# Optimization experiments

Hardware: AMD Instinct MI355X
Metric: run time of the kernel (lower is better)

Reference implementation:

```python
import jax, jax.numpy as jnp
import numpy as np

NEG_SLOPE = 0.01  # nn.LeakyReLU default
NUM_GRAPHS = 64


def leaky_relu(x):
    return jnp.where(x >= 0, x, NEG_SLOPE * x)


def gcn_conv(x, edge_index, W, b):
    """PyG GCNConv: add self-loops, symmetric norm, aggregate, + bias."""
    n = x.shape[0]
    h = x @ W  # [N, F]
    loop = jnp.arange(n, dtype=edge_index.dtype)
    src = jnp.concatenate([edge_index[0], loop])
    dst = jnp.concatenate([edge_index[1], loop])
    deg = jax.ops.segment_sum(jnp.ones_like(dst, dtype=h.dtype), dst, num_segments=n)
    dinv = jnp.where(deg > 0, deg ** -0.5, 0.0)
    norm = dinv[src] * dinv[dst]  # [E+N]
    msg = h[src] * norm[:, None]  # [E+N, F] dominant intermediate
    out = jax.ops.segment_sum(msg, dst, num_segments=n)
    return out + b


def gep(x, batch, num_graphs):
    """global mean pool over batch segment ids."""
    s = jax.ops.segment_sum(x, batch, num_segments=num_graphs)
    cnt = jax.ops.segment_sum(jnp.ones(x.shape[0], dtype=x.dtype), batch, num_segments=num_graphs)
    return s / jnp.maximum(cnt, 1.0)[:, None]


def setup_inputs() -> dict:
    key = jax.random.key(0)
    ks = jax.random.split(key, 16)
    N, E, F, D, B = 10000, 80000, 1024, 128, NUM_GRAPHS
    sc = 1.0 / np.sqrt(F)
    inp = {
        "pro1_x": jax.random.normal(ks[0], (N, F), jnp.float32),
        "pro1_edge_index": jax.random.randint(ks[1], (2, E), 0, N, jnp.int64),
        "pro1_batch": jnp.sort(jax.random.randint(ks[2], (N,), 0, B, jnp.int64)),
        "pro2_x": jax.random.normal(ks[3], (N, F), jnp.float32),
        "pro2_edge_index": jax.random.randint(ks[4], (2, E), 0, N, jnp.int64),
        "pro2_batch": jnp.sort(jax.random.randint(ks[5], (N,), 0, B, jnp.int64)),
        "mas1_straight": 0, "mas1_flipped": 0, "mas2_straight": 0, "mas2_flipped": 0,
        "conv1_W": jax.random.normal(ks[6], (F, F), jnp.float32) * sc,
        "conv1_b": jnp.zeros((F,), jnp.float32),
        "fc1_W": jax.random.normal(ks[7], (F, D), jnp.float32) * sc,
        "fc1_b": jnp.zeros((D,), jnp.float32),
        "conv2_W": jax.random.normal(ks[8], (F, F), jnp.float32) * sc,
        "conv2_b": jnp.zeros((F,), jnp.float32),
        "fc2_W": jax.random.normal(ks[9], (F, D), jnp.float32) * sc,
        "fc2_b": jnp.zeros((D,), jnp.float32),
        "final_W": jax.random.normal(ks[10], (2 * D, 1), jnp.float32) * (1.0 / np.sqrt(2 * D)),
        "final_b": jnp.zeros((1,), jnp.float32),
    }
    return inp


def reference(pro1_x, pro1_edge_index, pro1_batch, pro2_x, pro2_edge_index, pro2_batch,
              mas1_straight, mas1_flipped, mas2_straight, mas2_flipped,
              conv1_W, conv1_b, fc1_W, fc1_b, conv2_W, conv2_b, fc2_W, fc2_b,
              final_W, final_b):
    # branch 1 (dropout = identity at inference)
    x = leaky_relu(gcn_conv(pro1_x, pro1_edge_index, conv1_W, conv1_b))
    x = gep(x, pro1_batch, NUM_GRAPHS)
    x = leaky_relu(x @ fc1_W + fc1_b)
    # branch 2
    xt = leaky_relu(gcn_conv(pro2_x, pro2_edge_index, conv2_W, conv2_b))
    xt = gep(xt, pro2_batch, NUM_GRAPHS)
    xt = leaky_relu(xt @ fc2_W + fc2_b)
    combined = jnp.concatenate([x, xt], axis=1)  # [B, 256]
    return combined @ final_W + final_b  # [B, 1]
```

## Files before the change

### kernel.cpp

```cpp
#include <hip/hip_runtime.h>
#include <cstdint>
#include <cstddef>

#define FDIM 1024
#define DDIM 128
#define NGRAPH 64
#define FCH 8
#define QN 4
#define FILLB 320

#define AS1 __attribute__((address_space(1)))
#define AS3 __attribute__((address_space(3)))

typedef float f32x4 __attribute__((ext_vector_type(4)));
typedef short s16x8 __attribute__((ext_vector_type(8)));
typedef unsigned short u16x8 __attribute__((ext_vector_type(8)));

__device__ __forceinline__ unsigned short f2bf(float f) {
  unsigned int x = __float_as_uint(f);
  unsigned int r = (x + 0x7fffu + ((x >> 16) & 1u)) >> 16;
  return (unsigned short)r;
}
__device__ __forceinline__ float bflo(unsigned int v) {
  return __uint_as_float(v << 16);
}
__device__ __forceinline__ float bfhi(unsigned int v) {
  return __uint_as_float(v & 0xffff0000u);
}

__device__ __forceinline__ int lower_bound(const int* a, int n, int v) {
  int lo = 0, hi = n;
  while (lo < hi) {
    int mid = (lo + hi) >> 1;
    if (a[mid] < v) lo = mid + 1; else hi = mid;
  }
  return lo;
}

__global__ __launch_bounds__(256) void k_prep_cast(const int* __restrict__ ei1,
                                                   const int* __restrict__ ei2,
                                                   int* deg1, int* deg2,
                                                   const float4* __restrict__ x1,
                                                   const float4* __restrict__ x2,
                                                   const float* __restrict__ W1,
                                                   const float* __restrict__ W2,
                                                   u16x8* xb1, u16x8* xb2,
                                                   unsigned short* Wt1, unsigned short* Wt2,
                                                   int E, int n8, int gE, int nxb) {
  __shared__ unsigned short tile[64][65];
  int br = blockIdx.y;
  int x = blockIdx.x, t = threadIdx.x;
  if (x < gE) {
    const int* ei = br ? ei2 : ei1;
    int* deg = br ? deg2 : deg1;
    int i = x * 256 + t;
    if (i < E) atomicAdd(&deg[ei[E + i]], 1);
  } else if (x < gE + nxb) {
    const float4* xx = br ? x2 : x1;
    u16x8* xb = br ? xb2 : xb1;
    int i = (x - gE) * 256 + t;
    if (i < n8) {
      float4 v0 = xx[2 * i];
      float4 v1 = xx[2 * i + 1];
      u16x8 o;
      o[0] = f2bf(v0.x); o[1] = f2bf(v0.y); o[2] = f2bf(v0.z); o[3] = f2bf(v0.w);
      o[4] = f2bf(v1.x); o[5] = f2bf(v1.y); o[6] = f2bf(v1.z); o[7] = f2bf(v1.w);
      xb[i] = o;
    }
  } else {
    const float* W = br ? W2 : W1;
    unsigned short* Wt = br ? Wt2 : Wt1;
    int tid16 = x - gE - nxb;
    int kb = tid16 >> 4, nb = tid16 & 15;
    int tn = t & 63, tg = t >> 6;
    #pragma unroll
    for (int r = 0; r < 16; ++r) {
      int kk = tg * 16 + r;
      tile[kk][tn] = f2bf(W[(size_t)(kb * 64 + kk) * FDIM + nb * 64 + tn]);
    }
    __syncthreads();
    #pragma unroll
    for (int r = 0; r < 16; ++r) {
      int nn = tg * 16 + r;
      Wt[(size_t)(nb * 64 + nn) * FDIM + kb * 64 + tn] = tile[tn][nn];
    }
  }
}

#define SCAN_T 1024
#define SCAN_PER 16
__global__ __launch_bounds__(SCAN_T) void k_scan(const int* __restrict__ deg1,
                                                 const int* __restrict__ deg2,
                                                 int* off1, int* off2,
                                                 int* cur1, int* cur2,
                                                 float* dinv1, float* dinv2,
                                                 const int* __restrict__ batch1,
                                                 const int* __restrict__ batch2,
                                                 int* cnt1, int* gstart1,
                                                 int* cnt2, int* gstart2, int n) {
  if (blockIdx.x == 2) {
    int t = threadIdx.x;
    if (t < 128) {
      const int* batch = (t < NGRAPH) ? batch1 : batch2;
      int* cnt = (t < NGRAPH) ? cnt1 : cnt2;
      int* gstart = (t < NGRAPH) ? gstart1 : gstart2;
      int g = t & (NGRAPH - 1);
      int lo = lower_bound(batch, n, g);
      int hi = lower_bound(batch, n, g + 1);
      gstart[g] = lo;
      cnt[g] = hi - lo;
    }
    return;
  }
  const int* deg = blockIdx.x ? deg2 : deg1;
  int* off = blockIdx.x ? off2 : off1;
  int* cur = blockIdx.x ? cur2 : cur1;
  float* dinv = blockIdx.x ? dinv2 : dinv1;
  __shared__ int sums[SCAN_T];
  int t = threadIdx.x;
  int base = t * SCAN_PER;
  int local[SCAN_PER];
  int s = 0;
  #pragma unroll
  for (int i = 0; i < SCAN_PER; ++i) {
    int idx = base + i;
    int d = (idx < n) ? (deg[idx] + 1) : 0;
    local[i] = s;
    s += d;
    if (idx < n) dinv[idx] = rsqrtf((float)d);
  }
  sums[t] = s;
  __syncthreads();
  for (int o = 1; o < SCAN_T; o <<= 1) {
    int v = (t >= o) ? sums[t - o] : 0;
    __syncthreads();
    sums[t] += v;
    __syncthreads();
  }
  int basesum = (t > 0) ? sums[t - 1] : 0;
  #pragma unroll
  for (int i = 0; i < SCAN_PER; ++i) {
    int idx = base + i;
    if (idx < n) { int o = basesum + local[i]; off[idx] = o; cur[idx] = o; }
  }
  if (t == SCAN_T - 1) off[n] = sums[SCAN_T - 1];
}

__global__ __launch_bounds__(256, 3) void k_fill_gemm(const int* __restrict__ ei1,
                                                      const int* __restrict__ ei2,
                                                      int* cur1, int* cur2,
                                                      const float* __restrict__ dinv1,
                                                      const float* __restrict__ dinv2,
                                                      int* adjsrc1, int* adjsrc2,
                                                      float* adjw1, float* adjw2,
                                                      const unsigned short* __restrict__ A1,
                                                      const unsigned short* __restrict__ A2,
                                                      const unsigned short* __restrict__ B1,
                                                      const unsigned short* __restrict__ B2,
                                                      unsigned short* __restrict__ C1,
                                                      unsigned short* __restrict__ C2,
                                                      int E, int N, int M) {
  __shared__ unsigned short sm[8192];
  int br = blockIdx.y;
  if (blockIdx.x < FILLB) {
    const int* ei = br ? ei2 : ei1;
    int* cur = br ? cur2 : cur1;
    const float* dinv = br ? dinv2 : dinv1;
    int* adjsrc = br ? adjsrc2 : adjsrc1;
    float* adjw = br ? adjw2 : adjw1;
    int i = blockIdx.x * 256 + threadIdx.x;
    if (i < E) {
      int s = ei[i];
      int d = ei[E + i];
      int p = atomicAdd(&cur[d], 1);
      adjsrc[p] = s;
      adjw[p] = dinv[s] * dinv[d];
    }
    if (i < N) {
      int p = atomicAdd(&cur[i], 1);
      adjsrc[p] = i;
      adjw[p] = dinv[i] * dinv[i];
    }
    return;
  }
  const unsigned short* A = br ? A2 : A1;
  const unsigned short* Bt = br ? B2 : B1;
  unsigned short* C = br ? C2 : C1;
  const int K = FDIM;
  int tid = threadIdx.x;
  int w = tid >> 6, lane = tid & 63;
  int wm = w >> 1, wn = w & 1;

  int bx = blockIdx.x - FILLB;
  int per_xcd = (gridDim.x - FILLB) >> 3;
  int l = (bx & 7) * per_xcd + (bx >> 3);
  int m0 = (l >> 3) * 128;
  int n0 = (l & 7) * 128;

  int sub = lane >> 2;
  int kq = lane & 3;

  f32x4 acc[4][4];
  #pragma unroll
  for (int i = 0; i < 4; ++i)
    #pragma unroll
    for (int j = 0; j < 4; ++j)
      acc[i][j] = (f32x4){0.f, 0.f, 0.f, 0.f};

  for (int k0 = 0; k0 < K; k0 += 32) {
    #pragma unroll
    for (int j = 0; j < 2; ++j) {
      int chunk = w * 2 + j;
      int ra = m0 + chunk * 16 + sub;
      if (ra > M - 1) ra = M - 1;
      const unsigned short* ga = A + (size_t)ra * K + k0 + kq * 8;
      __builtin_amdgcn_global_load_lds((const AS1 unsigned int*)ga,
                                       (AS3 unsigned int*)&sm[chunk * 512], 16, 0, 0);
      int rb = n0 + chunk * 16 + sub;
      const unsigned short* gb = Bt + (size_t)rb * K + k0 + kq * 8;
      __builtin_amdgcn_global_load_lds((const AS1 unsigned int*)gb,
                                       (AS3 unsigned int*)&sm[4096 + chunk * 512], 16, 0, 0);
    }
    __syncthreads();
    s16x8 af[4], bfr[4];
    #pragma unroll
    for (int i = 0; i < 4; ++i) {
      int rowa = wm * 64 + i * 16 + (lane & 15);
      af[i] = *(const s16x8*)&sm[rowa * 32 + (lane >> 4) * 8];
      int rowb = wn * 64 + i * 16 + (lane & 15);
      bfr[i] = *(const s16x8*)&sm[4096 + rowb * 32 + (lane >> 4) * 8];
    }
    #pragma unroll
    for (int i = 0; i < 4; ++i)
      #pragma unroll
      for (int j = 0; j < 4; ++j)
        acc[i][j] = __builtin_amdgcn_mfma_f32_16x16x32_bf16(af[i], bfr[j], acc[i][j], 0, 0, 0);
    __syncthreads();
  }

  #pragma unroll
  for (int i = 0; i < 4; ++i) {
    int row_base = m0 + wm * 64 + i * 16 + (lane >> 4) * 4;
    #pragma unroll
    for (int j = 0; j < 4; ++j) {
      int col = n0 + wn * 64 + j * 16 + (lane & 15);
      #pragma unroll
      for (int r = 0; r < 4; ++r) {
        int row = row_base + r;
        if (row < M) C[(size_t)row * FDIM + col] = f2bf(acc[i][j][r]);
      }
    }
  }
}

__global__ __launch_bounds__(256) void k_aggpool(const unsigned short* __restrict__ h1,
                                                 const unsigned short* __restrict__ h2,
                                                 const int* __restrict__ off1,
                                                 const int* __restrict__ off2,
                                                 const int* __restrict__ adjsrc1,
                                                 const int* __restrict__ adjsrc2,
                                                 const float* __restrict__ adjw1,
                                                 const float* __restrict__ adjw2,
                                                 const float* __restrict__ bias1,
                                                 const float* __restrict__ bias2,
                                                 const int* __restrict__ cnt1,
                                                 const int* __restrict__ cnt2,
                                                 const int* __restrict__ gstart1,
                                                 const int* __restrict__ gstart2,
                                                 float* pool4_1, float* pool4_2) {
  int br = blockIdx.y;
  const unsigned short* h = br ? h2 : h1;
  const int* off = br ? off2 : off1;
  const int* adjsrc = br ? adjsrc2 : adjsrc1;
  const float* adjw = br ? adjw2 : adjw1;
  const float* bias = br ? bias2 : bias1;
  const int* cnt = br ? cnt2 : cnt1;
  const int* gstart = br ? gstart2 : gstart1;
  float* pool4 = br ? pool4_2 : pool4_1;

  int x = blockIdx.x;
  int chunk = x & (FCH - 1);
  int r = x >> 3;
  int g = r & (NGRAPH - 1);
  int q = r >> 6;

  int t = threadIdx.x;
  int grp = t >> 6, lane = t & 63;

  int n = cnt[g];
  int start = gstart[g];
  int per = (n + QN - 1) / QN;
  int v0 = start + q * per;
  int v1 = min(start + n, v0 + per);

  int colbase = chunk * 128 + lane * 2;
  const unsigned short* hc = h + colbase;
  float2 b2 = *(const float2*)(bias + colbase);
  float s0 = 0.f, s1 = 0.f;

  for (int v = v0 + grp; v < v1; v += 4) {
    int pb = off[v], pe = off[v + 1];
    float a0 = 0.f, a1 = 0.f;
    for (int pbb = pb; pbb < pe; pbb += 64) {
      int m = min(64, pe - pbb);
      int lp = pbb + ((lane < m) ? lane : (m - 1));
      int vs = adjsrc[lp];
      float vw = adjw[lp];
      int j = 0;
      for (; j + 4 <= m; j += 4) {
        int i0 = __shfl(vs, j),     i1 = __shfl(vs, j + 1);
        int i2 = __shfl(vs, j + 2), i3 = __shfl(vs, j + 3);
        float w0 = __shfl(vw, j),     w1 = __shfl(vw, j + 1);
        float w2 = __shfl(vw, j + 2), w3 = __shfl(vw, j + 3);
        unsigned int h0 = *(const unsigned int*)(hc + ((size_t)i0 << 10));
        unsigned int hv1 = *(const unsigned int*)(hc + ((size_t)i1 << 10));
        unsigned int hv2 = *(const unsigned int*)(hc + ((size_t)i2 << 10));
        unsigned int hv3 = *(const unsigned int*)(hc + ((size_t)i3 << 10));
        a0 += w0 * bflo(h0);  a1 += w0 * bfhi(h0);
        a0 += w1 * bflo(hv1); a1 += w1 * bfhi(hv1);
        a0 += w2 * bflo(hv2); a1 += w2 * bfhi(hv2);
        a0 += w3 * bflo(hv3); a1 += w3 * bfhi(hv3);
      }
      for (; j < m; ++j) {
        int i0 = __shfl(vs, j);
        float w0 = __shfl(vw, j);
        unsigned int h0 = *(const unsigned int*)(hc + ((size_t)i0 << 10));
        a0 += w0 * bflo(h0);
        a1 += w0 * bfhi(h0);
      }
    }
    a0 += b2.x; a1 += b2.y;
    s0 += (a0 >= 0.f) ? a0 : 0.01f * a0;
    s1 += (a1 >= 0.f) ? a1 : 0.01f * a1;
  }

  __shared__ float sm[4][128];
  sm[grp][lane * 2] = s0;
  sm[grp][lane * 2 + 1] = s1;
  __syncthreads();
  if (t < 128) {
    float sum = sm[0][t] + sm[1][t] + sm[2][t] + sm[3][t];
    float ic = 1.0f / fmaxf((float)n, 1.0f);
    pool4[((size_t)(q * NGRAPH + g)) * FDIM + chunk * 128 + t] = sum * ic;
  }
}

__global__ __launch_bounds__(256) void k_fc_final(const float* __restrict__ pool4_1,
                                                  const float* __restrict__ pool4_2,
                                                  const float* __restrict__ W1,
                                                  const float* __restrict__ W2,
                                                  const float* __restrict__ b1,
                                                  const float* __restrict__ b2,
                                                  const float* __restrict__ fW,
                                                  const float* __restrict__ fb,
                                                  float* __restrict__ out) {
  int g = blockIdx.x;
  int t = threadIdx.x;
  int half = t >> 7;
  int j = t & 127;
  const float* pool4 = half ? pool4_2 : pool4_1;
  const float* W = half ? W2 : W1;
  const float* b = half ? b2 : b1;
  __shared__ float xs[2][FDIM];
  for (int k = j; k < FDIM; k += DDIM) {
    float v = 0.f;
    #pragma unroll
    for (int q = 0; q < QN; ++q)
      v += pool4[((size_t)(q * NGRAPH + g)) * FDIM + k];
    xs[half][k] = v;
  }
  __syncthreads();
  float acc = b[j];
  for (int k = 0; k < FDIM; ++k) acc += xs[half][k] * W[(size_t)k * DDIM + j];
  acc = (acc >= 0.f) ? acc : 0.01f * acc;
  float c = acc * fW[half * DDIM + j];
  #pragma unroll
  for (int o = 32; o > 0; o >>= 1) c += __shfl_down(c, o);
  __shared__ float ws[4];
  if ((t & 63) == 0) ws[t >> 6] = c;
  __syncthreads();
  if (t == 0) out[g] = ws[0] + ws[1] + ws[2] + ws[3] + fb[0];
}

extern "C" void kernel_launch(void* const* d_in, const int* in_sizes, int n_in,
                              void* d_out, int out_size, void* d_ws, size_t ws_size,
                              hipStream_t stream) {
  const float* x1 = (const float*)d_in[0];
  const int* ei1 = (const int*)d_in[1];
  const int* batch1 = (const int*)d_in[2];
  const float* x2 = (const float*)d_in[3];
  const int* ei2 = (const int*)d_in[4];
  const int* batch2 = (const int*)d_in[5];
  const float* conv1_W = (const float*)d_in[10];
  const float* conv1_b = (const float*)d_in[11];
  const float* fc1_W = (const float*)d_in[12];
  const float* fc1_b = (const float*)d_in[13];
  const float* conv2_W = (const float*)d_in[14];
  const float* conv2_b = (const float*)d_in[15];
  const float* fc2_W = (const float*)d_in[16];
  const float* fc2_b = (const float*)d_in[17];
  const float* final_W = (const float*)d_in[18];
  const float* final_b = (const float*)d_in[19];
  float* out = (float*)d_out;

  const int N = in_sizes[2];
  const int E = in_sizes[1] / 2;
  const int A = E + N;

  size_t off_b = 0;
  auto alloc = [&](size_t bytes) -> void* {
    void* p = (char*)d_ws + off_b;
    off_b += (bytes + 255) & ~(size_t)255;
    return p;
  };
  unsigned short* xbf1 = (unsigned short*)alloc((size_t)N * FDIM * 2);
  unsigned short* xbf2 = (unsigned short*)alloc((size_t)N * FDIM * 2);
  unsigned short* hbf1 = (unsigned short*)alloc((size_t)N * FDIM * 2);
  unsigned short* hbf2 = (unsigned short*)alloc((size_t)N * FDIM * 2);
  unsigned short* Wt1 = (unsigned short*)alloc((size_t)FDIM * FDIM * 2);
  unsigned short* Wt2 = (unsigned short*)alloc((size_t)FDIM * FDIM * 2);
  int* deg1 = (int*)alloc(N * 4);
  int* deg2 = (int*)alloc(N * 4);
  int* cnt1 = (int*)alloc(NGRAPH * 4);
  int* cnt2 = (int*)alloc(NGRAPH * 4);
  int* gstart1 = (int*)alloc(NGRAPH * 4);
  int* gstart2 = (int*)alloc(NGRAPH * 4);
  int* off1 = (int*)alloc((N + 1) * 4);
  int* off2 = (int*)alloc((N + 1) * 4);
  int* cur1 = (int*)alloc(N * 4);
  int* cur2 = (int*)alloc(N * 4);
  float* dinv1 = (float*)alloc(N * 4);
  float* dinv2 = (float*)alloc(N * 4);
  int* adjsrc1 = (int*)alloc((size_t)A * 4);
  int* adjsrc2 = (int*)alloc((size_t)A * 4);
  float* adjw1 = (float*)alloc((size_t)A * 4);
  float* adjw2 = (float*)alloc((size_t)A * 4);
  float* pool4_1 = (float*)alloc((size_t)QN * NGRAPH * FDIM * 4);
  float* pool4_2 = (float*)alloc((size_t)QN * NGRAPH * FDIM * 4);

  const int T = 256;
  int gE = (E + T - 1) / T;
  int n8 = N * FDIM / 8;
  int nxb = (n8 + T - 1) / T;
  int mt = (N + 127) / 128;
  dim3 gPrepCast(gE + nxb + 256, 2);
  dim3 gFillGemm(FILLB + mt * 8, 2);
  dim3 gAgg(FCH * NGRAPH * QN, 2);

  hipMemsetAsync(deg1, 0, (size_t)N * 4, stream);
  hipMemsetAsync(deg2, 0, (size_t)N * 4, stream);
  k_prep_cast<<<gPrepCast, T, 0, stream>>>(ei1, ei2, deg1, deg2,
                                           (const float4*)x1, (const float4*)x2,
                                           conv1_W, conv2_W,
                                           (u16x8*)xbf1, (u16x8*)xbf2, Wt1, Wt2,
                                           E, n8, gE, nxb);
  k_scan<<<3, SCAN_T, 0, stream>>>(deg1, deg2, off1, off2, cur1, cur2, dinv1, dinv2,
                                   batch1, batch2, cnt1, gstart1, cnt2, gstart2, N);
  k_fill_gemm<<<gFillGemm, T, 0, stream>>>(ei1, ei2, cur1, cur2, dinv1, dinv2,
                                           adjsrc1, adjsrc2, adjw1, adjw2,
                                           xbf1, xbf2, Wt1, Wt2, hbf1, hbf2,
                                           E, N, N);
  k_aggpool<<<gAgg, T, 0, stream>>>(hbf1, hbf2, off1, off2, adjsrc1, adjsrc2,
                                    adjw1, adjw2, conv1_b, conv2_b,
                                    cnt1, cnt2, gstart1, gstart2, pool4_1, pool4_2);
  k_fc_final<<<NGRAPH, T, 0, stream>>>(pool4_1, pool4_2, fc1_W, fc2_W, fc1_b, fc2_b,
                                       final_W, final_b, out);
}
```

Before: 324.0 us.

## Triple-buffer GEMM LDS staging with swizzled layout and explicit waitcnt pipelining

```diff
diff --git a/kernel.cpp b/kernel.cpp
--- a/kernel.cpp
+++ b/kernel.cpp
@@ -160,7 +160,7 @@
                                                       unsigned short* __restrict__ C1,
                                                       unsigned short* __restrict__ C2,
                                                       int E, int N, int M) {
-  __shared__ unsigned short sm[8192];
+  __shared__ unsigned short sm[24576];
   int br = blockIdx.y;
   if (blockIdx.x < FILLB) {
     const int* ei = br ? ei2 : ei1;
@@ -197,8 +197,19 @@
   int m0 = (l >> 3) * 128;
   int n0 = (l & 7) * 128;
 
-  int sub = lane >> 2;
-  int kq = lane & 3;
+  int la = lane & 15, u4 = lane >> 4;
+
+  int rs = w * 32 + (lane >> 2);
+  int c16 = (lane & 3) ^ ((lane >> 3) & 3);
+  const unsigned short* gA0 = A + (size_t)min(m0 + rs, M - 1) * K + c16 * 8;
+  const unsigned short* gA1 = A + (size_t)min(m0 + rs + 16, M - 1) * K + c16 * 8;
+  const unsigned short* gB0 = Bt + (size_t)(n0 + rs) * K + c16 * 8;
+  const unsigned short* gB1 = Bt + (size_t)(n0 + rs + 16) * K + c16 * 8;
+  int lbA = w * 1024;
+
+  int sw = ((la >> 1) & 3) ^ u4;
+  unsigned raoff = (unsigned)((wm * 64 + la) * 32 + sw * 8);
+  unsigned rboff = (unsigned)(4096 + (wn * 64 + la) * 32 + sw * 8);
 
   f32x4 acc[4][4];
   #pragma unroll
@@ -207,36 +218,76 @@
     for (int j = 0; j < 4; ++j)
       acc[i][j] = (f32x4){0.f, 0.f, 0.f, 0.f};
 
-  for (int k0 = 0; k0 < K; k0 += 32) {
-    #pragma unroll
-    for (int j = 0; j < 2; ++j) {
-      int chunk = w * 2 + j;
-      int ra = m0 + chunk * 16 + sub;
-      if (ra > M - 1) ra = M - 1;
-      const unsigned short* ga = A + (size_t)ra * K + k0 + kq * 8;
-      __builtin_amdgcn_global_load_lds((const AS1 unsigned int*)ga,
-                                       (AS3 unsigned int*)&sm[chunk * 512], 16, 0, 0);
-      int rb = n0 + chunk * 16 + sub;
-      const unsigned short* gb = Bt + (size_t)rb * K + k0 + kq * 8;
-      __builtin_amdgcn_global_load_lds((const AS1 unsigned int*)gb,
-                                       (AS3 unsigned int*)&sm[4096 + chunk * 512], 16, 0, 0);
-    }
-    __syncthreads();
-    s16x8 af[4], bfr[4];
-    #pragma unroll
-    for (int i = 0; i < 4; ++i) {
-      int rowa = wm * 64 + i * 16 + (lane & 15);
-      af[i] = *(const s16x8*)&sm[rowa * 32 + (lane >> 4) * 8];
-      int rowb = wn * 64 + i * 16 + (lane & 15);
-      bfr[i] = *(const s16x8*)&sm[4096 + rowb * 32 + (lane >> 4) * 8];
-    }
-    #pragma unroll
-    for (int i = 0; i < 4; ++i)
-      #pragma unroll
-      for (int j = 0; j < 4; ++j)
-        acc[i][j] = __builtin_amdgcn_mfma_f32_16x16x32_bf16(af[i], bfr[j], acc[i][j], 0, 0, 0);
-    __syncthreads();
-  }
+  auto STAGE = [&](int bb, int kc) {
+    int kq = kc * 32;
+    int b0 = bb * 8192 + lbA;
+    __builtin_amdgcn_global_load_lds((const AS1 unsigned int*)(gA0 + kq),
+                                     (AS3 unsigned int*)&sm[b0], 16, 0, 0);
+    __builtin_amdgcn_global_load_lds((const AS1 unsigned int*)(gA1 + kq),
+                                     (AS3 unsigned int*)&sm[b0 + 512], 16, 0, 0);
+    __builtin_amdgcn_global_load_lds((const AS1 unsigned int*)(gB0 + kq),
+                                     (AS3 unsigned int*)&sm[b0 + 4096], 16, 0, 0);
+    __builtin_amdgcn_global_load_lds((const AS1 unsigned int*)(gB1 + kq),
+                                     (AS3 unsigned int*)&sm[b0 + 4096 + 512], 16, 0, 0);
+  };
+
+  auto COMPUTE = [&](int bb) {
+    const AS3 unsigned short* pa = (const AS3 unsigned short*)&sm[0] + bb * 8192 + raoff;
+    const AS3 unsigned short* pb = (const AS3 unsigned short*)&sm[0] + bb * 8192 + rboff;
+    s16x8 a0, a1, a2, a3, b0, b1, b2, b3;
+    asm volatile("ds_read_b128 %0, %1 offset:0"    : "=v"(a0) : "v"(pa));
+    asm volatile("ds_read_b128 %0, %1 offset:1024" : "=v"(a1) : "v"(pa));
+    asm volatile("ds_read_b128 %0, %1 offset:2048" : "=v"(a2) : "v"(pa));
+    asm volatile("ds_read_b128 %0, %1 offset:3072" : "=v"(a3) : "v"(pa));
+    asm volatile("ds_read_b128 %0, %1 offset:0"    : "=v"(b0) : "v"(pb));
+    asm volatile("ds_read_b128 %0, %1 offset:1024" : "=v"(b1) : "v"(pb));
+    asm volatile("ds_read_b128 %0, %1 offset:2048" : "=v"(b2) : "v"(pb));
+    asm volatile("ds_read_b128 %0, %1 offset:3072" : "=v"(b3) : "v"(pb));
+    asm volatile("s_waitcnt lgkmcnt(0)" ::: "memory");
+    __builtin_amdgcn_sched_barrier(0);
+    __builtin_amdgcn_s_setprio(1);
+    acc[0][0] = __builtin_amdgcn_mfma_f32_16x16x32_bf16(a0, b0, acc[0][0], 0, 0, 0);
+    acc[0][1] = __builtin_amdgcn_mfma_f32_16x16x32_bf16(a0, b1, acc[0][1], 0, 0, 0);
+    acc[0][2] = __builtin_amdgcn_mfma_f32_16x16x32_bf16(a0, b2, acc[0][2], 0, 0, 0);
+    acc[0][3] = __builtin_amdgcn_mfma_f32_16x16x32_bf16(a0, b3, acc[0][3], 0, 0, 0);
+    acc[1][0] = __builtin_amdgcn_mfma_f32_16x16x32_bf16(a1, b0, acc[1][0], 0, 0, 0);
+    acc[1][1] = __builtin_amdgcn_mfma_f32_16x16x32_bf16(a1, b1, acc[1][1], 0, 0, 0);
+    acc[1][2] = __builtin_amdgcn_mfma_f32_16x16x32_bf16(a1, b2, acc[1][2], 0, 0, 0);
+    acc[1][3] = __builtin_amdgcn_mfma_f32_16x16x32_bf16(a1, b3, acc[1][3], 0, 0, 0);
+    acc[2][0] = __builtin_amdgcn_mfma_f32_16x16x32_bf16(a2, b0, acc[2][0], 0, 0, 0);
+    acc[2][1] = __builtin_amdgcn_mfma_f32_16x16x32_bf16(a2, b1, acc[2][1], 0, 0, 0);
+    acc[2][2] = __builtin_amdgcn_mfma_f32_16x16x32_bf16(a2, b2, acc[2][2], 0, 0, 0);
+    acc[2][3] = __builtin_amdgcn_mfma_f32_16x16x32_bf16(a2, b3, acc[2][3], 0, 0, 0);
+    acc[3][0] = __builtin_amdgcn_mfma_f32_16x16x32_bf16(a3, b0, acc[3][0], 0, 0, 0);
+    acc[3][1] = __builtin_amdgcn_mfma_f32_16x16x32_bf16(a3, b1, acc[3][1], 0, 0, 0);
+    acc[3][2] = __builtin_amdgcn_mfma_f32_16x16x32_bf16(a3, b2, acc[3][2], 0, 0, 0);
+    acc[3][3] = __builtin_amdgcn_mfma_f32_16x16x32_bf16(a3, b3, acc[3][3], 0, 0, 0);
+    __builtin_amdgcn_s_setprio(0);
+  };
+
+  STAGE(0, 0);
+  STAGE(1, 1);
+  int sb = 2, cb = 0;
+  for (int kt = 0; kt < 30; ++kt) {
+    STAGE(sb, kt + 2);
+    asm volatile("s_waitcnt vmcnt(8)" ::: "memory");
+    __builtin_amdgcn_sched_barrier(0);
+    __builtin_amdgcn_s_barrier();
+    COMPUTE(cb);
+    __builtin_amdgcn_s_barrier();
+    sb = (sb == 2) ? 0 : sb + 1;
+    cb = (cb == 2) ? 0 : cb + 1;
+  }
+  asm volatile("s_waitcnt vmcnt(4)" ::: "memory");
+  __builtin_amdgcn_sched_barrier(0);
+  __builtin_amdgcn_s_barrier();
+  COMPUTE(cb);
+  __builtin_amdgcn_s_barrier();
+  cb = (cb == 2) ? 0 : cb + 1;
+  asm volatile("s_waitcnt vmcnt(0)" ::: "memory");
+  __builtin_amdgcn_sched_barrier(0);
+  __builtin_amdgcn_s_barrier();
+  COMPUTE(cb);
 
   #pragma unroll
   for (int i = 0; i < 4; ++i) {
```

New measurement: 317.1 us. 2.1% less time.
